# Optimization experiments

Measured on AMD Instinct MI355X. Metric: run time of the kernel, lower is better.

Reference implementation:

```python
import jax, jax.numpy as jnp
import numpy as np

INPUT_CHANNELS = 64
OUT_CHANNELS = 64
OUT_DIM = 4
IN_FEAT = INPUT_CHANNELS * OUT_DIM * 2   # 512
OUT_FEAT = OUT_CHANNELS * OUT_DIM        # 256
BATCH = 65536


def setup_inputs() -> dict:
    key = jax.random.key(0)
    k_x, k_w, k_b = jax.random.split(key, 3)
    x = jax.random.normal(k_x, (BATCH, IN_FEAT), dtype=jnp.float32)
    weight = jax.random.normal(k_w, (OUT_FEAT, IN_FEAT), dtype=jnp.float32)
    bias = jax.random.normal(k_b, (1, OUT_FEAT), dtype=jnp.float32)
    return {"x": x, "weight": weight, "bias": bias}


def reference(x, weight, bias) -> jnp.ndarray:
    # Original: (x[:, None] * weight).sum(-1) / sqrt(input_channels) + 0.1*bias
    # Mathematically identical to a GEMM: x @ weight.T
    scale = 1.0 / jnp.sqrt(jnp.asarray(INPUT_CHANNELS, dtype=x.dtype))
    out = jnp.einsum('bi,oi->bo', x, weight) * scale  # [B, out_feat]
    out = out + bias * 0.1
    return out
```

## Files before the change

kernel.cpp:

```cpp
#include <hip/hip_runtime.h>
#include <hip/hip_bf16.h>


typedef __bf16 bf16;
typedef __attribute__((ext_vector_type(8))) __bf16 bf16x8;
typedef __attribute__((ext_vector_type(4))) __bf16 bf16x4;
typedef __attribute__((ext_vector_type(4))) float f32x4;

#define BATCH_ 65536
#define KDIM   512
#define NDIM   256
#define NHALF  128
#define CHUNK_ROWS 16
#define CHUNKS 8
#define ROWS_PER_BLOCK (CHUNK_ROWS * CHUNKS)

__global__ __launch_bounds__(256) void wcvt_kernel(const float* __restrict__ w,
                                                   bf16* __restrict__ wb) {
    int i = (blockIdx.x * 256 + threadIdx.x) * 4;
    f32x4 v = *(const f32x4*)(w + i);
    bf16x4 o;
    o[0] = (bf16)(v.x * 0.125f);
    o[1] = (bf16)(v.y * 0.125f);
    o[2] = (bf16)(v.z * 0.125f);
    o[3] = (bf16)(v.w * 0.125f);
    *(bf16x4*)(wb + i) = o;
}

__device__ __forceinline__ void stage_issue(const float* xc, int tid, f32x4 (&r)[4]) {
#pragma unroll
    for (int i = 0; i < 4; ++i)
        r[i] = *(const f32x4*)((const char*)xc + i * 8192 + tid * 16);
}

__device__ __forceinline__ void stage_write(bf16* buf, int tid, const f32x4 (&r)[4]) {
#pragma unroll
    for (int i = 0; i < 4; ++i) {
        const int row = i * 4 + (tid >> 7);
        const int off = (tid & 127) * 8;
        const int phys = row * 1024 + (off ^ ((row & 7) << 4));
        bf16x4 o;
        o[0] = (bf16)r[i].x;
        o[1] = (bf16)r[i].y;
        o[2] = (bf16)r[i].z;
        o[3] = (bf16)r[i].w;
        *(bf16x4*)((char*)buf + phys) = o;
    }
}

__device__ __forceinline__ void compute_chunk(const bf16* buf, const bf16x8 (&wf)[16],
                                              int l16, int q, f32x4& acc) {
    acc = (f32x4)0.0f;
    const char* base = (const char*)buf + l16 * 1024;
    const int xo = (l16 & 7) << 4;
#pragma unroll
    for (int kc = 0; kc < 16; ++kc) {
        bf16x8 a = *(const bf16x8*)(base + ((kc * 64 + q * 16) ^ xo));
        acc = __builtin_amdgcn_mfma_f32_16x16x32_bf16(a, wf[kc], acc, 0, 0, 0);
    }
}

__device__ __forceinline__ void lds_barrier() {
    asm volatile("s_waitcnt lgkmcnt(0)" ::: "memory");
    __builtin_amdgcn_s_barrier();
    __builtin_amdgcn_sched_barrier(0);
}

__global__ __launch_bounds__(512, 4) void gemm_kernel(const float* __restrict__ x,
                                                      const bf16* __restrict__ wb,
                                                      const float* __restrict__ bias,
                                                      float* __restrict__ out) {
    __shared__ __align__(16) bf16 bufA[CHUNK_ROWS * KDIM];
    __shared__ __align__(16) bf16 bufB[CHUNK_ROWS * KDIM];

    const int tid  = threadIdx.x;
    const int lane = tid & 63;
    const int w    = tid >> 6;
    const int q    = lane >> 4;
    const int l16  = lane & 15;

    const int g    = blockIdx.x;
    const int half = (g >> 3) & 1;
    const long rb  = (long)((g & 7) | ((g >> 4) << 3));
    const int n0   = half * NHALF + w * 16;
    const long row_base = rb * ROWS_PER_BLOCK;

    bf16x8 wf[16];
#pragma unroll
    for (int kc = 0; kc < 16; ++kc)
        wf[kc] = *(const bf16x8*)(wb + (long)(n0 + l16) * KDIM + kc * 32 + q * 8);
    const float bv = 0.1f * bias[n0 + l16];

    const float* xblk = x + row_base * KDIM;

    f32x4 rA[4], rB[4];
    stage_issue(xblk, tid, rA);
    stage_issue(xblk + 1 * CHUNK_ROWS * KDIM, tid, rB);
    stage_write(bufA, tid, rA);
    lds_barrier();

    f32x4 acc;
#pragma unroll 1
    for (int t = 0; t < CHUNKS; t += 2) {
        if (t + 2 < CHUNKS)
            stage_issue(xblk + (long)(t + 2) * CHUNK_ROWS * KDIM, tid, rA);
        compute_chunk(bufA, wf, l16, q, acc);
        stage_write(bufB, tid, rB);
        lds_barrier();
        {
            const long row0 = row_base + (long)t * CHUNK_ROWS;
#pragma unroll
            for (int rr = 0; rr < 4; ++rr)
                out[(row0 + q * 4 + rr) * NDIM + n0 + l16] = acc[rr] + bv;
        }

        if (t + 3 < CHUNKS)
            stage_issue(xblk + (long)(t + 3) * CHUNK_ROWS * KDIM, tid, rB);
        compute_chunk(bufB, wf, l16, q, acc);
        if (t + 2 < CHUNKS)
            stage_write(bufA, tid, rA);
        lds_barrier();
        {
            const long row0 = row_base + (long)(t + 1) * CHUNK_ROWS;
#pragma unroll
            for (int rr = 0; rr < 4; ++rr)
                out[(row0 + q * 4 + rr) * NDIM + n0 + l16] = acc[rr] + bv;
        }
    }
}

extern "C" void kernel_launch(void* const* d_in, const int* in_sizes, int n_in,
                              void* d_out, int out_size, void* d_ws, size_t ws_size,
                              hipStream_t stream) {
    const float* x    = (const float*)d_in[0];
    const float* w    = (const float*)d_in[1];
    const float* bias = (const float*)d_in[2];
    float* out = (float*)d_out;
    bf16* wb   = (bf16*)d_ws;

    wcvt_kernel<<<(NDIM * KDIM) / (256 * 4), 256, 0, stream>>>(w, wb);
    gemm_kernel<<<(BATCH_ / ROWS_PER_BLOCK) * 2, 512, 0, stream>>>(x, wb, bias, out);
}
```

Baseline: 234.2 us.

## Stage GEMM output through LDS for 16-byte coalesced stores, shrink prefetch depth

```diff
diff --git a/kernel.cpp b/kernel.cpp
--- a/kernel.cpp
+++ b/kernel.cpp
@@ -14,6 +14,7 @@
 #define CHUNK_ROWS 16
 #define CHUNKS 8
 #define ROWS_PER_BLOCK (CHUNK_ROWS * CHUNKS)
+#define OPAD 132
 
 __global__ __launch_bounds__(256) void wcvt_kernel(const float* __restrict__ w,
                                                    bf16* __restrict__ wb) {
@@ -60,6 +61,24 @@
     }
 }
 
+__device__ __forceinline__ void owrite(float* ob, int w, int l16, int q,
+                                       const f32x4& acc) {
+    float* p = ob + (q * 4) * OPAD + w * 16 + l16;
+#pragma unroll
+    for (int rr = 0; rr < 4; ++rr)
+        p[rr * OPAD] = acc[rr];
+}
+
+__device__ __forceinline__ void ostore(const float* ob, float* __restrict__ out,
+                                       long row0, int half, int tid,
+                                       const f32x4& bvv) {
+    const int r2 = tid >> 5;
+    const int c4 = (tid & 31) * 4;
+    f32x4 v = *(const f32x4*)(ob + r2 * OPAD + c4);
+    v.x += bvv.x; v.y += bvv.y; v.z += bvv.z; v.w += bvv.w;
+    *(f32x4*)(out + (row0 + r2) * NDIM + half * NHALF + c4) = v;
+}
+
 __device__ __forceinline__ void lds_barrier() {
     asm volatile("s_waitcnt lgkmcnt(0)" ::: "memory");
     __builtin_amdgcn_s_barrier();
@@ -72,6 +91,8 @@
                                                       float* __restrict__ out) {
     __shared__ __align__(16) bf16 bufA[CHUNK_ROWS * KDIM];
     __shared__ __align__(16) bf16 bufB[CHUNK_ROWS * KDIM];
+    __shared__ __align__(16) float obuf0[CHUNK_ROWS * OPAD];
+    __shared__ __align__(16) float obuf1[CHUNK_ROWS * OPAD];
 
     const int tid  = threadIdx.x;
     const int lane = tid & 63;
@@ -89,43 +110,41 @@
 #pragma unroll
     for (int kc = 0; kc < 16; ++kc)
         wf[kc] = *(const bf16x8*)(wb + (long)(n0 + l16) * KDIM + kc * 32 + q * 8);
-    const float bv = 0.1f * bias[n0 + l16];
+
+    f32x4 bvv;
+    {
+        f32x4 b = *(const f32x4*)(bias + half * NHALF + (tid & 31) * 4);
+        bvv.x = 0.1f * b.x; bvv.y = 0.1f * b.y;
+        bvv.z = 0.1f * b.z; bvv.w = 0.1f * b.w;
+    }
 
     const float* xblk = x + row_base * KDIM;
 
-    f32x4 rA[4], rB[4];
-    stage_issue(xblk, tid, rA);
-    stage_issue(xblk + 1 * CHUNK_ROWS * KDIM, tid, rB);
-    stage_write(bufA, tid, rA);
+    f32x4 r[4];
+    stage_issue(xblk, tid, r);
+    stage_write(bufA, tid, r);
     lds_barrier();
 
     f32x4 acc;
 #pragma unroll 1
     for (int t = 0; t < CHUNKS; t += 2) {
+        if (t + 1 < CHUNKS)
+            stage_issue(xblk + (long)(t + 1) * CHUNK_ROWS * KDIM, tid, r);
+        compute_chunk(bufA, wf, l16, q, acc);
+        owrite(obuf0, w, l16, q, acc);
+        if (t + 1 < CHUNKS)
+            stage_write(bufB, tid, r);
+        lds_barrier();
+        ostore(obuf0, out, row_base + (long)t * CHUNK_ROWS, half, tid, bvv);
+
         if (t + 2 < CHUNKS)
-            stage_issue(xblk + (long)(t + 2) * CHUNK_ROWS * KDIM, tid, rA);
-        compute_chunk(bufA, wf, l16, q, acc);
-        stage_write(bufB, tid, rB);
+            stage_issue(xblk + (long)(t + 2) * CHUNK_ROWS * KDIM, tid, r);
+        compute_chunk(bufB, wf, l16, q, acc);
+        owrite(obuf1, w, l16, q, acc);
+        if (t + 2 < CHUNKS)
+            stage_write(bufA, tid, r);
         lds_barrier();
-        {
-            const long row0 = row_base + (long)t * CHUNK_ROWS;
-#pragma unroll
-            for (int rr = 0; rr < 4; ++rr)
-                out[(row0 + q * 4 + rr) * NDIM + n0 + l16] = acc[rr] + bv;
-        }
-
-        if (t + 3 < CHUNKS)
-            stage_issue(xblk + (long)(t + 3) * CHUNK_ROWS * KDIM, tid, rB);
-        compute_chunk(bufB, wf, l16, q, acc);
-        if (t + 2 < CHUNKS)
-            stage_write(bufA, tid, rA);
-        lds_barrier();
-        {
-            const long row0 = row_base + (long)(t + 1) * CHUNK_ROWS;
-#pragma unroll
-            for (int rr = 0; rr < 4; ++rr)
-                out[(row0 + q * 4 + rr) * NDIM + n0 + l16] = acc[rr] + bv;
-        }
+        ostore(obuf1, out, row_base + (long)(t + 1) * CHUNK_ROWS, half, tid, bvv);
     }
 }
 
```

Result: faster. 223.4 us (-4.6%).
